# Optimization experiments

Hardware: AMD Instinct MI355X
Metric: run time of the kernel (lower is better)

## Reference

```python
import jax, jax.numpy as jnp
import numpy as np

EPS = 1e-6  # torch.nn.PairwiseDistance default eps, added elementwise before the norm


def setup_inputs() -> dict:
    key = jax.random.key(0)
    k1, k2 = jax.random.split(key)
    source_prompt = jax.random.normal(k1, (50, 768), dtype=jnp.float32)      # [P, D]
    patch_embeds = jax.random.normal(k2, (1024, 197, 768), dtype=jnp.float32)  # [N, M, D]
    return {"source_prompt": source_prompt, "patch_embeds": patch_embeds, "src_task": 0}


def reference(source_prompt, patch_embeds, src_task):
    # torch: for each patch_embed [M,D], PairwiseDistance(src[:,None,:], pe[None,:,:])
    #   = ||src - pe + eps||_2 over last dim -> [P, M]; accumulate .mean(); divide by N.
    # lax.scan over N keeps peak memory at one [P, M, D] diff tensor, matching the
    # sequential reduction of the original loop without Python-level iteration.
    def step(acc, pe):                      # pe: [M, D]
        diff = source_prompt[:, None, :] - pe[None, :, :] + EPS   # [P, M, D]
        d = jnp.sqrt(jnp.sum(diff * diff, axis=-1))               # [P, M]
        return acc + jnp.mean(d), None

    total, _ = jax.lax.scan(step, jnp.zeros((), dtype=source_prompt.dtype), patch_embeds)
    return total / patch_embeds.shape[0]
```

## Files before the change

kernel.cpp:

```cpp
#include <hip/hip_runtime.h>


typedef __attribute__((ext_vector_type(8))) short bf16x8;
typedef __attribute__((ext_vector_type(4))) float f32x4;

#define D_DIM 768
#define NM_TOTAL 201728
#define COLS_PER_WG 128
#define NUM_WG (NM_TOTAL / COLS_PER_WG)

__device__ __forceinline__ unsigned short f2bf(float f) {
  unsigned int u = __float_as_uint(f);
  u += 0x7FFFu + ((u >> 16) & 1u);
  return (unsigned short)(u >> 16);
}

__global__ void prep_kernel(const float* __restrict__ src,
                            short* __restrict__ aW,
                            float* __restrict__ na) {
  const int r = blockIdx.x;
  const int lane = threadIdx.x;
  float sq = 0.f;
#pragma unroll
  for (int j = 0; j < 12; ++j) {
    const int c = lane + j * 64;
    float v = 0.f;
    if (r < 50) v = src[r * D_DIM + c] + 1e-6f;
    sq += v * v;
    aW[r * D_DIM + c] = (short)f2bf(v);
  }
#pragma unroll
  for (int m = 32; m >= 1; m >>= 1) sq += __shfl_xor(sq, m);
  if (lane == 0) na[r] = sq;
}

__global__ __launch_bounds__(512, 4) void dist_kernel(
    const float* __restrict__ pe,
    const short* __restrict__ aW,
    const float* __restrict__ na,
    float* __restrict__ partials) {
  const int tid  = threadIdx.x;
  const int wave = tid >> 6;
  const int lane = tid & 63;
  const int quad = lane >> 4;
  const int l16  = lane & 15;

  const int col = blockIdx.x * COLS_PER_WG + wave * 16 + l16;
  const float* brow = pe + (size_t)col * D_DIM + quad * 8;

  const short* a0p = aW + (size_t)(0 * 16 + l16) * D_DIM + quad * 8;
  const short* a1p = aW + (size_t)(1 * 16 + l16) * D_DIM + quad * 8;
  const short* a2p = aW + (size_t)(2 * 16 + l16) * D_DIM + quad * 8;
  const short* a3p = aW + (size_t)(3 * 16 + l16) * D_DIM + quad * 8;

  f32x4 acc0 = {0.f, 0.f, 0.f, 0.f};
  f32x4 acc1 = {0.f, 0.f, 0.f, 0.f};
  f32x4 acc2 = {0.f, 0.f, 0.f, 0.f};
  f32x4 acc3 = {0.f, 0.f, 0.f, 0.f};
  float nb = 0.f;

#pragma unroll 2
  for (int it = 0; it < 24; ++it) {
    const float4 f0 = *(const float4*)(brow + it * 32);
    const float4 f1 = *(const float4*)(brow + it * 32 + 4);

    bf16x8 af0 = *(const bf16x8*)(a0p + it * 32);
    bf16x8 af1 = *(const bf16x8*)(a1p + it * 32);
    bf16x8 af2 = *(const bf16x8*)(a2p + it * 32);
    bf16x8 af3 = *(const bf16x8*)(a3p + it * 32);

    nb = fmaf(f0.x, f0.x, nb); nb = fmaf(f0.y, f0.y, nb);
    nb = fmaf(f0.z, f0.z, nb); nb = fmaf(f0.w, f0.w, nb);
    nb = fmaf(f1.x, f1.x, nb); nb = fmaf(f1.y, f1.y, nb);
    nb = fmaf(f1.z, f1.z, nb); nb = fmaf(f1.w, f1.w, nb);

    union { bf16x8 v; unsigned short u[8]; } b;
    b.u[0] = f2bf(f0.x); b.u[1] = f2bf(f0.y);
    b.u[2] = f2bf(f0.z); b.u[3] = f2bf(f0.w);
    b.u[4] = f2bf(f1.x); b.u[5] = f2bf(f1.y);
    b.u[6] = f2bf(f1.z); b.u[7] = f2bf(f1.w);

    acc0 = __builtin_amdgcn_mfma_f32_16x16x32_bf16(af0, b.v, acc0, 0, 0, 0);
    acc1 = __builtin_amdgcn_mfma_f32_16x16x32_bf16(af1, b.v, acc1, 0, 0, 0);
    acc2 = __builtin_amdgcn_mfma_f32_16x16x32_bf16(af2, b.v, acc2, 0, 0, 0);
    acc3 = __builtin_amdgcn_mfma_f32_16x16x32_bf16(af3, b.v, acc3, 0, 0, 0);
  }

  nb += __shfl_xor(nb, 16);
  nb += __shfl_xor(nb, 32);

  float s = 0.f;
  {
    const float* accf;
    f32x4 accs[4] = {acc0, acc1, acc2, acc3};
#pragma unroll
    for (int t = 0; t < 4; ++t) {
#pragma unroll
      for (int r = 0; r < 4; ++r) {
        const int p = t * 16 + quad * 4 + r;
        if (p < 50) {
          const float c = accs[t][r];
          const float d2 = fmaxf(na[p] + nb - 2.f * c, 0.f);
          s += sqrtf(d2);
        }
      }
    }
    (void)accf;
  }

#pragma unroll
  for (int m = 32; m >= 1; m >>= 1) s += __shfl_xor(s, m);

  __shared__ float wsum[8];
  if (lane == 0) wsum[wave] = s;
  __syncthreads();
  if (tid == 0) {
    float t = 0.f;
#pragma unroll
    for (int i = 0; i < 8; ++i) t += wsum[i];
    partials[blockIdx.x] = t;
  }
}

__global__ void finalize_kernel(const float* __restrict__ partials,
                                float* __restrict__ out) {
  __shared__ float red[256];
  float s = 0.f;
  for (int i = threadIdx.x; i < NUM_WG; i += 256) s += partials[i];
  red[threadIdx.x] = s;
  __syncthreads();
  for (int step = 128; step >= 1; step >>= 1) {
    if (threadIdx.x < step) red[threadIdx.x] += red[threadIdx.x + step];
    __syncthreads();
  }
  if (threadIdx.x == 0) out[0] = red[0] * (1.0f / 10086400.0f);
}

extern "C" void kernel_launch(void* const* d_in, const int* in_sizes, int n_in,
                              void* d_out, int out_size, void* d_ws, size_t ws_size,
                              hipStream_t stream) {
  const float* src = (const float*)d_in[0];
  const float* pe  = (const float*)d_in[1];
  float* out = (float*)d_out;

  char* ws = (char*)d_ws;
  float* partials = (float*)ws;
  float* na       = (float*)(ws + 8192);
  short* aW       = (short*)(ws + 16384);

  prep_kernel<<<64, 64, 0, stream>>>(src, aW, na);
  dist_kernel<<<NUM_WG, 512, 0, stream>>>(pe, aW, na, partials);
  finalize_kernel<<<1, 256, 0, stream>>>(partials, out);
}
```

Measured before the change: 913.3 us.

## Stage patch rows through double-buffered LDS with direct global-to-LDS loads

Instead of each lane reading strided float4s straight from global memory, each workgroup now streams 64-wide K chunks of its 128 patch rows into a double-buffered LDS tile using global_load_lds, with an XOR swizzle to avoid bank conflicts. The next chunk is prefetched while MFMAs run on the current one. The aim is fully coalesced global reads and overlap of memory with compute on this bandwidth-bound kernel. The cost is 64KB of LDS per workgroup, which may cut occupancy below the launch-bounds target, plus one barrier per chunk.

```diff
diff --git a/kernel.cpp b/kernel.cpp
--- a/kernel.cpp
+++ b/kernel.cpp
@@ -8,6 +8,8 @@
 #define NM_TOTAL 201728
 #define COLS_PER_WG 128
 #define NUM_WG (NM_TOTAL / COLS_PER_WG)
+#define KC 64
+#define NCHUNK (D_DIM / KC)
 
 __device__ __forceinline__ unsigned short f2bf(float f) {
   unsigned int u = __float_as_uint(f);
@@ -39,19 +41,23 @@
     const short* __restrict__ aW,
     const float* __restrict__ na,
     float* __restrict__ partials) {
+  __shared__ __attribute__((aligned(16))) float buf[2][COLS_PER_WG * KC];
+
   const int tid  = threadIdx.x;
   const int wave = tid >> 6;
   const int lane = tid & 63;
   const int quad = lane >> 4;
   const int l16  = lane & 15;
+  const int colL = wave * 16 + l16;
+  const int col0 = blockIdx.x * COLS_PER_WG;
 
-  const int col = blockIdx.x * COLS_PER_WG + wave * 16 + l16;
-  const float* brow = pe + (size_t)col * D_DIM + quad * 8;
+  const int s_sub = lane >> 4;
+  const int cpos  = lane & 15;
 
-  const short* a0p = aW + (size_t)(0 * 16 + l16) * D_DIM + quad * 8;
-  const short* a1p = aW + (size_t)(1 * 16 + l16) * D_DIM + quad * 8;
-  const short* a2p = aW + (size_t)(2 * 16 + l16) * D_DIM + quad * 8;
-  const short* a3p = aW + (size_t)(3 * 16 + l16) * D_DIM + quad * 8;
+  const short* a0p = aW + (size_t)(0 * 16 + l16) * D_DIM;
+  const short* a1p = aW + (size_t)(1 * 16 + l16) * D_DIM;
+  const short* a2p = aW + (size_t)(2 * 16 + l16) * D_DIM;
+  const short* a3p = aW + (size_t)(3 * 16 + l16) * D_DIM;
 
   f32x4 acc0 = {0.f, 0.f, 0.f, 0.f};
   f32x4 acc1 = {0.f, 0.f, 0.f, 0.f};
@@ -59,31 +65,63 @@
   f32x4 acc3 = {0.f, 0.f, 0.f, 0.f};
   float nb = 0.f;
 
-#pragma unroll 2
-  for (int it = 0; it < 24; ++it) {
-    const float4 f0 = *(const float4*)(brow + it * 32);
-    const float4 f1 = *(const float4*)(brow + it * 32 + 4);
+#pragma unroll
+  for (int r = 0; r < 4; ++r) {
+    const int cl   = wave * 16 + r * 4 + s_sub;
+    const int cdat = cpos ^ (cl & 15);
+    const float* g = pe + (size_t)(col0 + cl) * D_DIM + cdat * 4;
+    __builtin_amdgcn_global_load_lds(
+        (const __attribute__((address_space(1))) void*)g,
+        (__attribute__((address_space(3))) void*)&buf[0][(wave * 16 + r * 4) * KC],
+        16, 0, 0);
+  }
+  __syncthreads();
 
-    bf16x8 af0 = *(const bf16x8*)(a0p + it * 32);
-    bf16x8 af1 = *(const bf16x8*)(a1p + it * 32);
-    bf16x8 af2 = *(const bf16x8*)(a2p + it * 32);
-    bf16x8 af3 = *(const bf16x8*)(a3p + it * 32);
+  for (int it = 0; it < NCHUNK; ++it) {
+    const int cur = it & 1;
+    if (it + 1 < NCHUNK) {
+#pragma unroll
+      for (int r = 0; r < 4; ++r) {
+        const int cl   = wave * 16 + r * 4 + s_sub;
+        const int cdat = cpos ^ (cl & 15);
+        const float* g = pe + (size_t)(col0 + cl) * D_DIM + (it + 1) * KC + cdat * 4;
+        __builtin_amdgcn_global_load_lds(
+            (const __attribute__((address_space(1))) void*)g,
+            (__attribute__((address_space(3))) void*)&buf[cur ^ 1][(wave * 16 + r * 4) * KC],
+            16, 0, 0);
+      }
+    }
 
-    nb = fmaf(f0.x, f0.x, nb); nb = fmaf(f0.y, f0.y, nb);
-    nb = fmaf(f0.z, f0.z, nb); nb = fmaf(f0.w, f0.w, nb);
-    nb = fmaf(f1.x, f1.x, nb); nb = fmaf(f1.y, f1.y, nb);
-    nb = fmaf(f1.z, f1.z, nb); nb = fmaf(f1.w, f1.w, nb);
+    const float* bufc = buf[cur];
+#pragma unroll
+    for (int s = 0; s < 2; ++s) {
+      const int kbase = it * KC + s * 32;
+      const int P0 = s * 8 + quad * 2;
+      const f32x4 u0 = *(const f32x4*)&bufc[colL * KC + ((P0 ^ l16) << 2)];
+      const f32x4 u1 = *(const f32x4*)&bufc[colL * KC + (((P0 + 1) ^ l16) << 2)];
 
-    union { bf16x8 v; unsigned short u[8]; } b;
-    b.u[0] = f2bf(f0.x); b.u[1] = f2bf(f0.y);
-    b.u[2] = f2bf(f0.z); b.u[3] = f2bf(f0.w);
-    b.u[4] = f2bf(f1.x); b.u[5] = f2bf(f1.y);
-    b.u[6] = f2bf(f1.z); b.u[7] = f2bf(f1.w);
+      nb = fmaf(u0.x, u0.x, nb); nb = fmaf(u0.y, u0.y, nb);
+      nb = fmaf(u0.z, u0.z, nb); nb = fmaf(u0.w, u0.w, nb);
+      nb = fmaf(u1.x, u1.x, nb); nb = fmaf(u1.y, u1.y, nb);
+      nb = fmaf(u1.z, u1.z, nb); nb = fmaf(u1.w, u1.w, nb);
 
-    acc0 = __builtin_amdgcn_mfma_f32_16x16x32_bf16(af0, b.v, acc0, 0, 0, 0);
-    acc1 = __builtin_amdgcn_mfma_f32_16x16x32_bf16(af1, b.v, acc1, 0, 0, 0);
-    acc2 = __builtin_amdgcn_mfma_f32_16x16x32_bf16(af2, b.v, acc2, 0, 0, 0);
-    acc3 = __builtin_amdgcn_mfma_f32_16x16x32_bf16(af3, b.v, acc3, 0, 0, 0);
+      union { bf16x8 v; unsigned short u[8]; } b;
+      b.u[0] = f2bf(u0.x); b.u[1] = f2bf(u0.y);
+      b.u[2] = f2bf(u0.z); b.u[3] = f2bf(u0.w);
+      b.u[4] = f2bf(u1.x); b.u[5] = f2bf(u1.y);
+      b.u[6] = f2bf(u1.z); b.u[7] = f2bf(u1.w);
+
+      bf16x8 af0 = *(const bf16x8*)(a0p + kbase + quad * 8);
+      bf16x8 af1 = *(const bf16x8*)(a1p + kbase + quad * 8);
+      bf16x8 af2 = *(const bf16x8*)(a2p + kbase + quad * 8);
+      bf16x8 af3 = *(const bf16x8*)(a3p + kbase + quad * 8);
+
+      acc0 = __builtin_amdgcn_mfma_f32_16x16x32_bf16(af0, b.v, acc0, 0, 0, 0);
+      acc1 = __builtin_amdgcn_mfma_f32_16x16x32_bf16(af1, b.v, acc1, 0, 0, 0);
+      acc2 = __builtin_amdgcn_mfma_f32_16x16x32_bf16(af2, b.v, acc2, 0, 0, 0);
+      acc3 = __builtin_amdgcn_mfma_f32_16x16x32_bf16(af3, b.v, acc3, 0, 0, 0);
+    }
+    __syncthreads();
   }
 
   nb += __shfl_xor(nb, 16);
@@ -91,7 +129,6 @@
 
   float s = 0.f;
   {
-    const float* accf;
     f32x4 accs[4] = {acc0, acc1, acc2, acc3};
 #pragma unroll
     for (int t = 0; t < 4; ++t) {
@@ -105,13 +142,12 @@
         }
       }
     }
-    (void)accf;
   }
 
 #pragma unroll
   for (int m = 32; m >= 1; m >>= 1) s += __shfl_xor(s, m);
 
-  __shared__ float wsum[8];
+  float* wsum = (float*)buf;
   if (lane == 0) wsum[wave] = s;
   __syncthreads();
   if (tid == 0) {
```

New measurement: 843.6 us. 1.08x faster.
